# Performance work log

Measured on AMD Instinct MI355X. Metric: run time of the kernel, lower is better.

Reference implementation:

```python
import jax, jax.numpy as jnp
import numpy as np

COMPRESSION = 2

def setup_inputs() -> dict:
    key = jax.random.key(0)
    k = jax.random.split(key, 5)
    B, H, W, C, Ci = 8, 56, 56, 256, 128
    return {
        "x": jax.random.normal(k[0], (B, H, W, C), dtype=jnp.float32),
        "w_theta": jax.random.normal(k[1], (C, Ci), dtype=jnp.float32) * (2.0 / C) ** 0.5,
        "w_phi": jax.random.normal(k[2], (C, Ci), dtype=jnp.float32) * (2.0 / C) ** 0.5,
        "w_g": jax.random.normal(k[3], (C, Ci), dtype=jnp.float32) * (2.0 / C) ** 0.5,
        "w_final": jax.random.normal(k[4], (Ci, C), dtype=jnp.float32) * (2.0 / Ci) ** 0.5,
    }

def _maxpool1d(z, pool):
    # z: [B, N, Ci]; non-overlapping max pool along N (Keras MaxPool1D default stride=pool)
    B, N, Ci = z.shape
    return z[:, : (N // pool) * pool].reshape(B, N // pool, pool, Ci).max(axis=2)

def reference(x, w_theta, w_phi, w_g, w_final):
    B, H, W, C = x.shape
    Ci = w_theta.shape[1]
    N = H * W
    xf = x.reshape(B, N, C)
    # 1x1 convs == per-position matmuls
    theta = xf @ w_theta                      # [B, N, Ci]
    phi = _maxpool1d(xf @ w_phi, COMPRESSION)  # [B, N/2, Ci]
    g = _maxpool1d(xf @ w_g, COMPRESSION)      # [B, N/2, Ci]
    f = jnp.einsum('bnc,bmc->bnm', theta, phi)  # [B, N, N/2]
    f = jax.nn.softmax(f, axis=-1)
    y = jnp.einsum('bnm,bmc->bnc', f, g)        # [B, N, Ci]
    z = y @ w_final                              # [B, N, C]
    return x + z.reshape(B, H, W, C)
```

## Files before the change

kernel.cpp:

```cpp
#include <hip/hip_runtime.h>

typedef _Float16 f16x8 __attribute__((ext_vector_type(8)));
typedef short s16x4 __attribute__((ext_vector_type(4)));
typedef float f32x4 __attribute__((ext_vector_type(4)));

#define MFMA_K32(a, b, c) __builtin_amdgcn_mfma_f32_16x16x32_f16(a, b, c, 0, 0, 0)
#define MFMA_BF(a, b, c)  __builtin_amdgcn_mfma_f32_16x16x16bf16_1k(a, b, c, 0, 0, 0)


__device__ __forceinline__ f16x8 ld8f(const float* __restrict__ p) {
    f32x4 a = *(const f32x4*)p;
    f32x4 b = *(const f32x4*)(p + 4);
    f16x8 r;
    r[0] = (_Float16)a[0]; r[1] = (_Float16)a[1];
    r[2] = (_Float16)a[2]; r[3] = (_Float16)a[3];
    r[4] = (_Float16)b[0]; r[5] = (_Float16)b[1];
    r[6] = (_Float16)b[2]; r[7] = (_Float16)b[3];
    return r;
}
__device__ __forceinline__ unsigned f2bf_rne(float f) {
    unsigned u = __float_as_uint(f);
    return (u + 0x7FFFu + ((u >> 16) & 1u)) >> 16;
}
__device__ __forceinline__ int bfpack_rtz(float lo, float hi) {
    return (int)((__float_as_uint(hi) & 0xFFFF0000u) | (__float_as_uint(lo) >> 16));
}

__global__ void k_prep(const float* __restrict__ wt, const float* __restrict__ wp,
                       const float* __restrict__ wg, const float* __restrict__ wf,
                       _Float16* __restrict__ wt_f, _Float16* __restrict__ wf_f) {
    int i = blockIdx.x * 256 + threadIdx.x;
    int w = i >> 15, idx = i & 32767;
    if (w < 3) {
        const float* src = (w == 0) ? wt : (w == 1) ? wp : wg;
        int k = idx >> 7, n = idx & 127;
        int ct = n >> 4, tt = n & 15, kc = k >> 5, qq = (k >> 3) & 3, jj = k & 7;
        wt_f[((w * 8 + ct) * 8 + kc) * 512 + (qq * 16 + tt) * 8 + jj] = (_Float16)src[idx];
    } else {
        int k = idx >> 8, n = idx & 255;
        int cb = n >> 7, ct = (n >> 4) & 7, tt = n & 15;
        int kc = k >> 5, qq = (k >> 3) & 3, jj = k & 7;
        wf_f[((cb * 8 + ct) * 4 + kc) * 512 + (qq * 16 + tt) * 8 + jj] = (_Float16)wf[idx];
    }
}

__global__ __launch_bounds__(128) void k_proj(
    const float* __restrict__ x,
    const _Float16* __restrict__ wt_f,
    _Float16* __restrict__ theta_f,
    _Float16* __restrict__ phi_f,
    short* __restrict__ g_f)
{
    const int r0   = blockIdx.x * 32;
    const int wave = threadIdx.x >> 6;
    const int lane = threadIdx.x & 63;
    const int q = lane >> 4, t = lane & 15;

    const int mrow = r0 + wave * 16 + t;
    f16x8 af[8];
#pragma unroll
    for (int kc = 0; kc < 8; ++kc)
        af[kc] = ld8f(x + mrow * 256 + kc * 32 + q * 8);

    const f32x4 zero = {0.f, 0.f, 0.f, 0.f};
    f32x4 acc[3][8];
#pragma unroll
    for (int w = 0; w < 3; ++w)
#pragma unroll
        for (int ct = 0; ct < 8; ++ct) acc[w][ct] = zero;

#pragma unroll
    for (int w = 0; w < 3; ++w)
#pragma unroll
        for (int ct = 0; ct < 8; ++ct) {
            const _Float16* Wc = wt_f + ((w * 8 + ct) * 8) * 512 + lane * 8;
#pragma unroll
            for (int kc = 0; kc < 8; ++kc)
                acc[w][ct] = MFMA_K32(af[kc], *(const f16x8*)(Wc + kc * 512), acc[w][ct]);
        }

    _Float16* tb = theta_f + (blockIdx.x * 2 + wave) * 2048;
#pragma unroll
    for (int ct = 0; ct < 8; ++ct) {
        const int off = (ct >> 1) * 512 + ((ct & 1) * 2 + (t >> 3)) * 128 + (t & 7);
#pragma unroll
        for (int r = 0; r < 4; ++r)
            tb[off + (q * 4 + r) * 8] = (_Float16)acc[0][ct][r];
    }

    const int b     = blockIdx.x / 98;
    const int mIdx  = blockIdx.x % 98;
    const int chunk = mIdx >> 1;
    const int h     = mIdx & 1;
    const int ttp   = wave * 8 + q * 2;

    _Float16* pcb = phi_f + (b * 49 + chunk) * 4096;
#pragma unroll
    for (int ct = 0; ct < 8; ++ct) {
        const int kc = ct >> 1;
        const int qq = (ct & 1) * 2 + (t >> 3);
        const int j  = t & 7;
        const int off = (h * 4 + kc) * 512 + (qq * 16 + ttp) * 8 + j;
        pcb[off]     = (_Float16)fmaxf(acc[1][ct][0], acc[1][ct][1]);
        pcb[off + 8] = (_Float16)fmaxf(acc[1][ct][2], acc[1][ct][3]);
    }

    short* gcb = g_f + (b * 49 + chunk) * 4096;
    const int qv  = wave * 2 + (q >> 1);
    const int jj0 = (q & 1) * 2;
#pragma unroll
    for (int ct = 0; ct < 8; ++ct) {
        unsigned lo = f2bf_rne(fmaxf(acc[2][ct][0], acc[2][ct][1]));
        unsigned hi = f2bf_rne(fmaxf(acc[2][ct][2], acc[2][ct][3]));
        *(unsigned*)(gcb + ct * 512 + (qv * 16 + t) * 8 + h * 4 + jj0) = lo | (hi << 16);
    }
}

__global__ __launch_bounds__(256) void k_attn(
    const _Float16* __restrict__ theta_f,
    const _Float16* __restrict__ phi_f,
    const short* __restrict__ g_f,
    _Float16* __restrict__ y_f)
{
    const int blk  = blockIdx.x;
    const int b    = blk & 7;
    const int blkm = blk >> 3;
    const int wave = threadIdx.x >> 6;
    const int lane = threadIdx.x & 63;
    const int q = lane >> 4, t = lane & 15;

    __shared__ __align__(16) _Float16 kv[2][8192];

    const int tIdx = b * 196 + blkm * 4 + wave;
    const _Float16* ph = phi_f + b * 200704;
    const _Float16* gt = (const _Float16*)(g_f + b * 200704);

    f16x8 qf[4];
#pragma unroll
    for (int kc = 0; kc < 4; ++kc)
        qf[kc] = *(const f16x8*)(theta_f + tIdx * 2048 + kc * 512 + lane * 8);

    const f32x4 zero = {0.f, 0.f, 0.f, 0.f};
    f32x4 o[8];
#pragma unroll
    for (int ct = 0; ct < 8; ++ct) o[ct] = zero;
    float lsum = 0.f;
    const float L2E = 1.44269504f, SHIFT = 104.0f;

    const _Float16* src0 = (wave < 2) ? (ph + wave * 2048) : (gt + (wave - 2) * 2048);
    const int doff = wave * 2048;

    f16x8 sr[4];
#pragma unroll
    for (int j = 0; j < 4; ++j)
        sr[j] = *(const f16x8*)(src0 + j * 512 + lane * 8);
#pragma unroll
    for (int j = 0; j < 4; ++j)
        *(f16x8*)(&kv[0][doff + j * 512 + lane * 8]) = sr[j];
    __syncthreads();

    for (int i = 0; i < 49; ++i) {
        if (i + 1 < 49) {
            const _Float16* s = src0 + (i + 1) * 4096;
#pragma unroll
            for (int j = 0; j < 4; ++j)
                sr[j] = *(const f16x8*)(s + j * 512 + lane * 8);
        }

        const _Float16* buf = &kv[i & 1][0];
        f32x4 st0 = zero, st1 = zero;
#pragma unroll
        for (int kc = 0; kc < 4; ++kc) {
            f16x8 a0 = *(const f16x8*)(buf + kc * 512 + lane * 8);
            f16x8 a1 = *(const f16x8*)(buf + (4 + kc) * 512 + lane * 8);
            st0 = MFMA_K32(a0, qf[kc], st0);
            st1 = MFMA_K32(a1, qf[kc], st1);
        }

        f32x4 p0, p1;
#pragma unroll
        for (int r = 0; r < 4; ++r) {
            p0[r] = exp2f(st0[r] * L2E - SHIFT);
            p1[r] = exp2f(st1[r] * L2E - SHIFT);
        }
        lsum += ((p0[0] + p0[1]) + (p0[2] + p0[3]))
              + ((p1[0] + p1[1]) + (p1[2] + p1[3]));
        union { int i2[2]; s16x4 v; } u0, u1;
        u0.i2[0] = bfpack_rtz(p0[0], p0[1]);
        u0.i2[1] = bfpack_rtz(p0[2], p0[3]);
        u1.i2[0] = bfpack_rtz(p1[0], p1[1]);
        u1.i2[1] = bfpack_rtz(p1[2], p1[3]);

#pragma unroll
        for (int ct = 0; ct < 8; ++ct) {
            union { f16x8 f; s16x4 s[2]; } uv;
            uv.f = *(const f16x8*)(buf + 4096 + ct * 512 + lane * 8);
            o[ct] = MFMA_BF(u0.v, uv.s[0], o[ct]);
            o[ct] = MFMA_BF(u1.v, uv.s[1], o[ct]);
        }

        if (i + 1 < 49) {
            _Float16* d = &kv[(i + 1) & 1][doff];
#pragma unroll
            for (int j = 0; j < 4; ++j)
                *(f16x8*)(d + j * 512 + lane * 8) = sr[j];
        }
        __syncthreads();
    }

    float lf = lsum;
    lf += __shfl_xor(lf, 16);
    lf += __shfl_xor(lf, 32);
    float inv[4];
#pragma unroll
    for (int r = 0; r < 4; ++r) inv[r] = 1.0f / __shfl(lf, q * 4 + r);

    _Float16* yb = y_f + tIdx * 2048;
#pragma unroll
    for (int ct = 0; ct < 8; ++ct) {
        const int off = (ct >> 1) * 512 + (2 * (ct & 1) + (t >> 3)) * 128 + (t & 7);
#pragma unroll
        for (int r = 0; r < 4; ++r)
            yb[off + (4 * q + r) * 8] = (_Float16)(o[ct][r] * inv[r]);
    }
}

__global__ __launch_bounds__(256) void k_final(
    const _Float16* __restrict__ y_f,
    const _Float16* __restrict__ wf_f,
    const float* __restrict__ x,
    float* __restrict__ out)
{
    const int r0   = blockIdx.x * 64;
    const int cb   = blockIdx.y;
    const int wave = threadIdx.x >> 6;
    const int lane = threadIdx.x & 63;
    const int q = lane >> 4, t = lane & 15;

    __shared__ float t_lds[4][16][132];

    const int tile = blockIdx.x * 4 + wave;
    f16x8 af[4];
#pragma unroll
    for (int kc = 0; kc < 4; ++kc)
        af[kc] = *(const f16x8*)(y_f + tile * 2048 + kc * 512 + lane * 8);

    const f32x4 zero = {0.f, 0.f, 0.f, 0.f};
    f32x4 acc[8];
#pragma unroll
    for (int ct = 0; ct < 8; ++ct) acc[ct] = zero;
#pragma unroll
    for (int ct = 0; ct < 8; ++ct) {
        const _Float16* Wc = wf_f + ((cb * 8 + ct) * 4) * 512 + lane * 8;
#pragma unroll
        for (int kc = 0; kc < 4; ++kc)
            acc[ct] = MFMA_K32(af[kc], *(const f16x8*)(Wc + kc * 512), acc[ct]);
    }

#pragma unroll
    for (int ct = 0; ct < 8; ++ct)
#pragma unroll
        for (int r = 0; r < 4; ++r)
            t_lds[wave][q * 4 + r][ct * 16 + t] = acc[ct][r];

    const int R0 = r0 + wave * 16;
#pragma unroll
    for (int p = 0; p < 4; ++p) {
        const int rr = p * 4 + q;
        const int c  = t * 8;
        f32x4 v0 = *(const f32x4*)&t_lds[wave][rr][c];
        f32x4 v1 = *(const f32x4*)&t_lds[wave][rr][c + 4];
        const float* xp = x + (R0 + rr) * 256 + cb * 128 + c;
        float* op = out + (R0 + rr) * 256 + cb * 128 + c;
        v0 += *(const f32x4*)xp;
        v1 += *(const f32x4*)(xp + 4);
        *(f32x4*)op = v0;
        *(f32x4*)(op + 4) = v1;
    }
}

extern "C" void kernel_launch(void* const* d_in, const int* in_sizes, int n_in,
                              void* d_out, int out_size, void* d_ws, size_t ws_size,
                              hipStream_t stream) {
    const float* x  = (const float*)d_in[0];
    const float* wt = (const float*)d_in[1];
    const float* wp = (const float*)d_in[2];
    const float* wg = (const float*)d_in[3];
    const float* wf = (const float*)d_in[4];
    float* out = (float*)d_out;

    _Float16* ws      = (_Float16*)d_ws;
    _Float16* wt_f    = ws;
    _Float16* wf_f    = ws + 98304;
    _Float16* theta_f = ws + 131072;
    _Float16* phi_f   = ws + 3342336;
    short*    g_f     = (short*)(ws + 4947968);
    _Float16* y_f     = ws + 6553600;

    k_prep <<<dim3(512),    256, 0, stream>>>(wt, wp, wg, wf, wt_f, wf_f);
    k_proj <<<dim3(784),    128, 0, stream>>>(x, wt_f, theta_f, phi_f, g_f);
    k_attn <<<dim3(392),    256, 0, stream>>>(theta_f, phi_f, g_f, y_f);
    k_final<<<dim3(392, 2), 256, 0, stream>>>(y_f, wf_f, x, out);
}
```

Baseline: 159.6 us.

## Fuse output projection into attention with single-wave blocks holding four query tiles

The attention kernel now runs one wave per block that processes four query tiles. K/V fragments are loaded straight from global memory into registers with software double-buffering, which replaces the shared-memory staging and barriers. The final projection plus residual is fused into the attention epilogue using a transposed f16 weight layout, so the y intermediate buffer and the separate k_final launch go away. The cost is a block count of only 392 single-wave blocks, which leaves many CUs underused. Register pressure is also very high (128 accumulator registers for o plus the q fragments), so spills and latency exposure are a risk.

Result: slower. 186.4 us (+16.8%).

```diff
diff --git a/kernel.cpp b/kernel.cpp
--- a/kernel.cpp
+++ b/kernel.cpp
@@ -1,11 +1,13 @@
 #include <hip/hip_runtime.h>
 
 typedef _Float16 f16x8 __attribute__((ext_vector_type(8)));
+typedef _Float16 f16x4 __attribute__((ext_vector_type(4)));
 typedef short s16x4 __attribute__((ext_vector_type(4)));
 typedef float f32x4 __attribute__((ext_vector_type(4)));
 
 #define MFMA_K32(a, b, c) __builtin_amdgcn_mfma_f32_16x16x32_f16(a, b, c, 0, 0, 0)
 #define MFMA_BF(a, b, c)  __builtin_amdgcn_mfma_f32_16x16x16bf16_1k(a, b, c, 0, 0, 0)
+#define MFMA_F16(a, b, c) __builtin_amdgcn_mfma_f32_16x16x16f16(a, b, c, 0, 0, 0)
 
 
 __device__ __forceinline__ f16x8 ld8f(const float* __restrict__ p) {
@@ -28,7 +30,7 @@
 
 __global__ void k_prep(const float* __restrict__ wt, const float* __restrict__ wp,
                        const float* __restrict__ wg, const float* __restrict__ wf,
-                       _Float16* __restrict__ wt_f, _Float16* __restrict__ wf_f) {
+                       _Float16* __restrict__ wt_f, _Float16* __restrict__ wfT_f) {
     int i = blockIdx.x * 256 + threadIdx.x;
     int w = i >> 15, idx = i & 32767;
     if (w < 3) {
@@ -38,9 +40,9 @@
         wt_f[((w * 8 + ct) * 8 + kc) * 512 + (qq * 16 + tt) * 8 + jj] = (_Float16)src[idx];
     } else {
         int k = idx >> 8, n = idx & 255;
-        int cb = n >> 7, ct = (n >> 4) & 7, tt = n & 15;
-        int kc = k >> 5, qq = (k >> 3) & 3, jj = k & 7;
-        wf_f[((cb * 8 + ct) * 4 + kc) * 512 + (qq * 16 + tt) * 8 + jj] = (_Float16)wf[idx];
+        int ct = n >> 4, tt = n & 15;
+        int kc2 = k >> 4, qq = (k >> 2) & 3, jj = k & 3;
+        wfT_f[ct * 2048 + (qq * 16 + tt) * 32 + kc2 * 4 + jj] = (_Float16)wf[idx];
     }
 }
 
@@ -116,166 +118,123 @@
     }
 }
 
-__global__ __launch_bounds__(256) void k_attn(
+#define LOADKV(DST, SRC) { _Pragma("unroll") \
+    for (int j = 0; j < 8; ++j) DST[j] = *(const f16x8*)((SRC) + j * 512 + lane * 8); }
+
+#define QKSM(PH) { \
+    f32x4 st0[4], st1[4]; \
+    _Pragma("unroll") for (int m = 0; m < 4; ++m) { st0[m] = zero; st1[m] = zero; } \
+    _Pragma("unroll") for (int kc = 0; kc < 4; ++kc) \
+      _Pragma("unroll") for (int m = 0; m < 4; ++m) { \
+        st0[m] = MFMA_K32(PH[kc],     qf[m][kc], st0[m]); \
+        st1[m] = MFMA_K32(PH[4 + kc], qf[m][kc], st1[m]); } \
+    _Pragma("unroll") for (int m = 0; m < 4; ++m) { \
+      f32x4 p0, p1; \
+      _Pragma("unroll") for (int r = 0; r < 4; ++r) { \
+        p0[r] = exp2f(st0[m][r] * L2E - SHIFT); \
+        p1[r] = exp2f(st1[m][r] * L2E - SHIFT); } \
+      lsum[m] += ((p0[0] + p0[1]) + (p0[2] + p0[3])) \
+               + ((p1[0] + p1[1]) + (p1[2] + p1[3])); \
+      u[m][0].i2[0] = bfpack_rtz(p0[0], p0[1]); \
+      u[m][0].i2[1] = bfpack_rtz(p0[2], p0[3]); \
+      u[m][1].i2[0] = bfpack_rtz(p1[0], p1[1]); \
+      u[m][1].i2[1] = bfpack_rtz(p1[2], p1[3]); } }
+
+#define PV(AG) { \
+    _Pragma("unroll") for (int ct = 0; ct < 8; ++ct) { \
+      union { f16x8 f; s16x4 s[2]; } uv; uv.f = AG[ct]; \
+      _Pragma("unroll") for (int m = 0; m < 4; ++m) { \
+        o[m][ct] = MFMA_BF(uv.s[0], u[m][0].v, o[m][ct]); \
+        o[m][ct] = MFMA_BF(uv.s[1], u[m][1].v, o[m][ct]); } } }
+
+__global__ __launch_bounds__(64, 1) void k_attn(
     const _Float16* __restrict__ theta_f,
     const _Float16* __restrict__ phi_f,
     const short* __restrict__ g_f,
-    _Float16* __restrict__ y_f)
+    const _Float16* __restrict__ wfT_f,
+    const float* __restrict__ x,
+    float* __restrict__ out)
 {
     const int blk  = blockIdx.x;
     const int b    = blk & 7;
     const int blkm = blk >> 3;
-    const int wave = threadIdx.x >> 6;
     const int lane = threadIdx.x & 63;
     const int q = lane >> 4, t = lane & 15;
 
-    __shared__ __align__(16) _Float16 kv[2][8192];
-
-    const int tIdx = b * 196 + blkm * 4 + wave;
+    const int tIdx0 = b * 196 + blkm * 4;
     const _Float16* ph = phi_f + b * 200704;
     const _Float16* gt = (const _Float16*)(g_f + b * 200704);
 
-    f16x8 qf[4];
-#pragma unroll
-    for (int kc = 0; kc < 4; ++kc)
-        qf[kc] = *(const f16x8*)(theta_f + tIdx * 2048 + kc * 512 + lane * 8);
+    f16x8 qf[4][4];
+#pragma unroll
+    for (int m = 0; m < 4; ++m)
+#pragma unroll
+        for (int kc = 0; kc < 4; ++kc)
+            qf[m][kc] = *(const f16x8*)(theta_f + (tIdx0 + m) * 2048 + kc * 512 + lane * 8);
 
     const f32x4 zero = {0.f, 0.f, 0.f, 0.f};
-    f32x4 o[8];
-#pragma unroll
-    for (int ct = 0; ct < 8; ++ct) o[ct] = zero;
-    float lsum = 0.f;
+    f32x4 o[4][8];
+#pragma unroll
+    for (int m = 0; m < 4; ++m)
+#pragma unroll
+        for (int ct = 0; ct < 8; ++ct) o[m][ct] = zero;
+    float lsum[4] = {0.f, 0.f, 0.f, 0.f};
+    union ubf { int i2[2]; s16x4 v; } u[4][2];
     const float L2E = 1.44269504f, SHIFT = 104.0f;
 
-    const _Float16* src0 = (wave < 2) ? (ph + wave * 2048) : (gt + (wave - 2) * 2048);
-    const int doff = wave * 2048;
-
-    f16x8 sr[4];
-#pragma unroll
-    for (int j = 0; j < 4; ++j)
-        sr[j] = *(const f16x8*)(src0 + j * 512 + lane * 8);
-#pragma unroll
-    for (int j = 0; j < 4; ++j)
-        *(f16x8*)(&kv[0][doff + j * 512 + lane * 8]) = sr[j];
-    __syncthreads();
-
-    for (int i = 0; i < 49; ++i) {
-        if (i + 1 < 49) {
-            const _Float16* s = src0 + (i + 1) * 4096;
-#pragma unroll
-            for (int j = 0; j < 4; ++j)
-                sr[j] = *(const f16x8*)(s + j * 512 + lane * 8);
+    f16x8 phA[8], phB[8], ag[8];
+    LOADKV(phA, ph);
+
+#pragma unroll 1
+    for (int i = 0; i < 48; i += 2) {
+        LOADKV(ag, gt + i * 4096);
+        QKSM(phA);
+        LOADKV(phB, ph + (i + 1) * 4096);
+        PV(ag);
+        LOADKV(ag, gt + (i + 1) * 4096);
+        QKSM(phB);
+        LOADKV(phA, ph + (i + 2) * 4096);
+        PV(ag);
+    }
+    LOADKV(ag, gt + 48 * 4096);
+    QKSM(phA);
+    PV(ag);
+
+    float inv[4];
+#pragma unroll
+    for (int m = 0; m < 4; ++m) {
+        float lf = lsum[m];
+        lf += __shfl_xor(lf, 16);
+        lf += __shfl_xor(lf, 32);
+        inv[m] = 1.0f / lf;
+    }
+
+    f16x4 yf[4][8];
+#pragma unroll
+    for (int m = 0; m < 4; ++m)
+#pragma unroll
+        for (int ct = 0; ct < 8; ++ct)
+#pragma unroll
+            for (int r = 0; r < 4; ++r)
+                yf[m][ct][r] = (_Float16)(o[m][ct][r] * inv[m]);
+
+    const int row0 = tIdx0 * 16;
+    for (int ctile = 0; ctile < 16; ++ctile) {
+        union { f16x8 v8; f16x4 v4[2]; } w[4];
+#pragma unroll
+        for (int p = 0; p < 4; ++p)
+            w[p].v8 = *(const f16x8*)(wfT_f + ctile * 2048 + lane * 32 + p * 8);
+#pragma unroll
+        for (int m = 0; m < 4; ++m) {
+            f32x4 acc = zero;
+#pragma unroll
+            for (int kc2 = 0; kc2 < 8; ++kc2)
+                acc = MFMA_F16(w[kc2 >> 1].v4[kc2 & 1], yf[m][kc2], acc);
+            const int row = row0 + m * 16 + t;
+            const int col = ctile * 16 + q * 4;
+            f32x4 xv = *(const f32x4*)(x + row * 256 + col);
+            *(f32x4*)(out + row * 256 + col) = acc + xv;
         }
-
-        const _Float16* buf = &kv[i & 1][0];
-        f32x4 st0 = zero, st1 = zero;
-#pragma unroll
-        for (int kc = 0; kc < 4; ++kc) {
-            f16x8 a0 = *(const f16x8*)(buf + kc * 512 + lane * 8);
-            f16x8 a1 = *(const f16x8*)(buf + (4 + kc) * 512 + lane * 8);
-            st0 = MFMA_K32(a0, qf[kc], st0);
-            st1 = MFMA_K32(a1, qf[kc], st1);
-        }
-
-        f32x4 p0, p1;
-#pragma unroll
-        for (int r = 0; r < 4; ++r) {
-            p0[r] = exp2f(st0[r] * L2E - SHIFT);
-            p1[r] = exp2f(st1[r] * L2E - SHIFT);
-        }
-        lsum += ((p0[0] + p0[1]) + (p0[2] + p0[3]))
-              + ((p1[0] + p1[1]) + (p1[2] + p1[3]));
-        union { int i2[2]; s16x4 v; } u0, u1;
-        u0.i2[0] = bfpack_rtz(p0[0], p0[1]);
-        u0.i2[1] = bfpack_rtz(p0[2], p0[3]);
-        u1.i2[0] = bfpack_rtz(p1[0], p1[1]);
-        u1.i2[1] = bfpack_rtz(p1[2], p1[3]);
-
-#pragma unroll
-        for (int ct = 0; ct < 8; ++ct) {
-            union { f16x8 f; s16x4 s[2]; } uv;
-            uv.f = *(const f16x8*)(buf + 4096 + ct * 512 + lane * 8);
-            o[ct] = MFMA_BF(u0.v, uv.s[0], o[ct]);
-            o[ct] = MFMA_BF(u1.v, uv.s[1], o[ct]);
-        }
-
-        if (i + 1 < 49) {
-            _Float16* d = &kv[(i + 1) & 1][doff];
-#pragma unroll
-            for (int j = 0; j < 4; ++j)
-                *(f16x8*)(d + j * 512 + lane * 8) = sr[j];
-        }
-        __syncthreads();
-    }
-
-    float lf = lsum;
-    lf += __shfl_xor(lf, 16);
-    lf += __shfl_xor(lf, 32);
-    float inv[4];
-#pragma unroll
-    for (int r = 0; r < 4; ++r) inv[r] = 1.0f / __shfl(lf, q * 4 + r);
-
-    _Float16* yb = y_f + tIdx * 2048;
-#pragma unroll
-    for (int ct = 0; ct < 8; ++ct) {
-        const int off = (ct >> 1) * 512 + (2 * (ct & 1) + (t >> 3)) * 128 + (t & 7);
-#pragma unroll
-        for (int r = 0; r < 4; ++r)
-            yb[off + (4 * q + r) * 8] = (_Float16)(o[ct][r] * inv[r]);
-    }
-}
-
-__global__ __launch_bounds__(256) void k_final(
-    const _Float16* __restrict__ y_f,
-    const _Float16* __restrict__ wf_f,
-    const float* __restrict__ x,
-    float* __restrict__ out)
-{
-    const int r0   = blockIdx.x * 64;
-    const int cb   = blockIdx.y;
-    const int wave = threadIdx.x >> 6;
-    const int lane = threadIdx.x & 63;
-    const int q = lane >> 4, t = lane & 15;
-
-    __shared__ float t_lds[4][16][132];
-
-    const int tile = blockIdx.x * 4 + wave;
-    f16x8 af[4];
-#pragma unroll
-    for (int kc = 0; kc < 4; ++kc)
-        af[kc] = *(const f16x8*)(y_f + tile * 2048 + kc * 512 + lane * 8);
-
-    const f32x4 zero = {0.f, 0.f, 0.f, 0.f};
-    f32x4 acc[8];
-#pragma unroll
-    for (int ct = 0; ct < 8; ++ct) acc[ct] = zero;
-#pragma unroll
-    for (int ct = 0; ct < 8; ++ct) {
-        const _Float16* Wc = wf_f + ((cb * 8 + ct) * 4) * 512 + lane * 8;
-#pragma unroll
-        for (int kc = 0; kc < 4; ++kc)
-            acc[ct] = MFMA_K32(af[kc], *(const f16x8*)(Wc + kc * 512), acc[ct]);
-    }
-
-#pragma unroll
-    for (int ct = 0; ct < 8; ++ct)
-#pragma unroll
-        for (int r = 0; r < 4; ++r)
-            t_lds[wave][q * 4 + r][ct * 16 + t] = acc[ct][r];
-
-    const int R0 = r0 + wave * 16;
-#pragma unroll
-    for (int p = 0; p < 4; ++p) {
-        const int rr = p * 4 + q;
-        const int c  = t * 8;
-        f32x4 v0 = *(const f32x4*)&t_lds[wave][rr][c];
-        f32x4 v1 = *(const f32x4*)&t_lds[wave][rr][c + 4];
-        const float* xp = x + (R0 + rr) * 256 + cb * 128 + c;
-        float* op = out + (R0 + rr) * 256 + cb * 128 + c;
-        v0 += *(const f32x4*)xp;
-        v1 += *(const f32x4*)(xp + 4);
-        *(f32x4*)op = v0;
-        *(f32x4*)(op + 4) = v1;
     }
 }
 
@@ -291,14 +250,12 @@
 
     _Float16* ws      = (_Float16*)d_ws;
     _Float16* wt_f    = ws;
-    _Float16* wf_f    = ws + 98304;
+    _Float16* wfT_f   = ws + 98304;
     _Float16* theta_f = ws + 131072;
     _Float16* phi_f   = ws + 3342336;
     short*    g_f     = (short*)(ws + 4947968);
-    _Float16* y_f     = ws + 6553600;
-
-    k_prep <<<dim3(512),    256, 0, stream>>>(wt, wp, wg, wf, wt_f, wf_f);
-    k_proj <<<dim3(784),    128, 0, stream>>>(x, wt_f, theta_f, phi_f, g_f);
-    k_attn <<<dim3(392),    256, 0, stream>>>(theta_f, phi_f, g_f, y_f);
-    k_final<<<dim3(392, 2), 256, 0, stream>>>(y_f, wf_f, x, out);
-}
+
+    k_prep<<<dim3(512), 256, 0, stream>>>(wt, wp, wg, wf, wt_f, wfT_f);
+    k_proj<<<dim3(784), 128, 0, stream>>>(x, wt_f, theta_f, phi_f, g_f);
+    k_attn<<<dim3(392),  64, 0, stream>>>(theta_f, phi_f, g_f, wfT_f, x, out);
+}
```

## Fuse final projection and residual into attention kernel; split projection per weight

Applied to the files above, without the earlier changes.

The final 1x1 projection and residual add move into the end of the attention kernel. The PV MFMA operands are swapped so the normalized output tile already sits in registers in the B-operand layout, and it is multiplied by a transposed f16 w_final. This removes the y intermediate round trip through global memory and one kernel launch. The projection kernel also now assigns one weight (theta, phi or g) per wave instead of all three, giving three times as many waves with fewer accumulators each. The risks are that the attention kernel's tail gets longer and runs with only 392 blocks, and that x is reloaded with 16-byte row-strided accesses.

New measurement: 160.4 us. About the same (+0.5%).

```diff
diff --git a/kernel.cpp b/kernel.cpp
--- a/kernel.cpp
+++ b/kernel.cpp
@@ -1,11 +1,13 @@
 #include <hip/hip_runtime.h>
 
 typedef _Float16 f16x8 __attribute__((ext_vector_type(8)));
+typedef _Float16 f16x4 __attribute__((ext_vector_type(4)));
 typedef short s16x4 __attribute__((ext_vector_type(4)));
 typedef float f32x4 __attribute__((ext_vector_type(4)));
 
 #define MFMA_K32(a, b, c) __builtin_amdgcn_mfma_f32_16x16x32_f16(a, b, c, 0, 0, 0)
 #define MFMA_BF(a, b, c)  __builtin_amdgcn_mfma_f32_16x16x16bf16_1k(a, b, c, 0, 0, 0)
+#define MFMA_F16(a, b, c) __builtin_amdgcn_mfma_f32_16x16x16f16(a, b, c, 0, 0, 0)
 
 
 __device__ __forceinline__ f16x8 ld8f(const float* __restrict__ p) {
@@ -28,7 +30,7 @@
 
 __global__ void k_prep(const float* __restrict__ wt, const float* __restrict__ wp,
                        const float* __restrict__ wg, const float* __restrict__ wf,
-                       _Float16* __restrict__ wt_f, _Float16* __restrict__ wf_f) {
+                       _Float16* __restrict__ wt_f, _Float16* __restrict__ wfT_f) {
     int i = blockIdx.x * 256 + threadIdx.x;
     int w = i >> 15, idx = i & 32767;
     if (w < 3) {
@@ -38,81 +40,85 @@
         wt_f[((w * 8 + ct) * 8 + kc) * 512 + (qq * 16 + tt) * 8 + jj] = (_Float16)src[idx];
     } else {
         int k = idx >> 8, n = idx & 255;
-        int cb = n >> 7, ct = (n >> 4) & 7, tt = n & 15;
-        int kc = k >> 5, qq = (k >> 3) & 3, jj = k & 7;
-        wf_f[((cb * 8 + ct) * 4 + kc) * 512 + (qq * 16 + tt) * 8 + jj] = (_Float16)wf[idx];
-    }
-}
-
-__global__ __launch_bounds__(128) void k_proj(
+        int ct = n >> 4, tt = n & 15;
+        int kc2 = k >> 4, qq = (k >> 2) & 3, jj = k & 3;
+        wfT_f[ct * 2048 + (qq * 16 + tt) * 32 + kc2 * 4 + jj] = (_Float16)wf[idx];
+    }
+}
+
+__global__ __launch_bounds__(256) void k_proj(
     const float* __restrict__ x,
     const _Float16* __restrict__ wt_f,
     _Float16* __restrict__ theta_f,
     _Float16* __restrict__ phi_f,
     short* __restrict__ g_f)
 {
-    const int r0   = blockIdx.x * 32;
-    const int wave = threadIdx.x >> 6;
+    const int u    = blockIdx.x * 4 + (threadIdx.x >> 6);
     const int lane = threadIdx.x & 63;
     const int q = lane >> 4, t = lane & 15;
 
-    const int mrow = r0 + wave * 16 + t;
+    const int tt = u / 3;
+    const int w  = u - tt * 3;
+
+    const int mrow = tt * 16 + t;
     f16x8 af[8];
 #pragma unroll
     for (int kc = 0; kc < 8; ++kc)
         af[kc] = ld8f(x + mrow * 256 + kc * 32 + q * 8);
 
     const f32x4 zero = {0.f, 0.f, 0.f, 0.f};
-    f32x4 acc[3][8];
-#pragma unroll
-    for (int w = 0; w < 3; ++w)
-#pragma unroll
-        for (int ct = 0; ct < 8; ++ct) acc[w][ct] = zero;
-
-#pragma unroll
-    for (int w = 0; w < 3; ++w)
-#pragma unroll
-        for (int ct = 0; ct < 8; ++ct) {
-            const _Float16* Wc = wt_f + ((w * 8 + ct) * 8) * 512 + lane * 8;
-#pragma unroll
-            for (int kc = 0; kc < 8; ++kc)
-                acc[w][ct] = MFMA_K32(af[kc], *(const f16x8*)(Wc + kc * 512), acc[w][ct]);
-        }
-
-    _Float16* tb = theta_f + (blockIdx.x * 2 + wave) * 2048;
+    f32x4 acc[8];
+#pragma unroll
+    for (int ct = 0; ct < 8; ++ct) acc[ct] = zero;
+
 #pragma unroll
     for (int ct = 0; ct < 8; ++ct) {
-        const int off = (ct >> 1) * 512 + ((ct & 1) * 2 + (t >> 3)) * 128 + (t & 7);
-#pragma unroll
-        for (int r = 0; r < 4; ++r)
-            tb[off + (q * 4 + r) * 8] = (_Float16)acc[0][ct][r];
-    }
-
-    const int b     = blockIdx.x / 98;
-    const int mIdx  = blockIdx.x % 98;
-    const int chunk = mIdx >> 1;
-    const int h     = mIdx & 1;
-    const int ttp   = wave * 8 + q * 2;
-
-    _Float16* pcb = phi_f + (b * 49 + chunk) * 4096;
-#pragma unroll
-    for (int ct = 0; ct < 8; ++ct) {
-        const int kc = ct >> 1;
-        const int qq = (ct & 1) * 2 + (t >> 3);
-        const int j  = t & 7;
-        const int off = (h * 4 + kc) * 512 + (qq * 16 + ttp) * 8 + j;
-        pcb[off]     = (_Float16)fmaxf(acc[1][ct][0], acc[1][ct][1]);
-        pcb[off + 8] = (_Float16)fmaxf(acc[1][ct][2], acc[1][ct][3]);
-    }
-
-    short* gcb = g_f + (b * 49 + chunk) * 4096;
-    const int qv  = wave * 2 + (q >> 1);
-    const int jj0 = (q & 1) * 2;
-#pragma unroll
-    for (int ct = 0; ct < 8; ++ct) {
-        unsigned lo = f2bf_rne(fmaxf(acc[2][ct][0], acc[2][ct][1]));
-        unsigned hi = f2bf_rne(fmaxf(acc[2][ct][2], acc[2][ct][3]));
-        *(unsigned*)(gcb + ct * 512 + (qv * 16 + t) * 8 + h * 4 + jj0) = lo | (hi << 16);
+        const _Float16* Wc = wt_f + ((w * 8 + ct) * 8) * 512 + lane * 8;
+#pragma unroll
+        for (int kc = 0; kc < 8; ++kc)
+            acc[ct] = MFMA_K32(af[kc], *(const f16x8*)(Wc + kc * 512), acc[ct]);
+    }
+
+    if (w == 0) {
+        _Float16* tb = theta_f + tt * 2048;
+#pragma unroll
+        for (int ct = 0; ct < 8; ++ct) {
+            const int off = (ct >> 1) * 512 + ((ct & 1) * 2 + (t >> 3)) * 128 + (t & 7);
+#pragma unroll
+            for (int r = 0; r < 4; ++r)
+                tb[off + (q * 4 + r) * 8] = (_Float16)acc[ct][r];
+        }
+        return;
+    }
+
+    const int b     = tt / 196;
+    const int tl    = tt - b * 196;
+    const int chunk = tl >> 2;
+    const int sub   = tl & 3;
+    const int h     = sub >> 1;
+
+    if (w == 1) {
+        const int ttp = (sub & 1) * 8 + q * 2;
+        _Float16* pcb = phi_f + (b * 49 + chunk) * 4096;
+#pragma unroll
+        for (int ct = 0; ct < 8; ++ct) {
+            const int kc = ct >> 1;
+            const int qq = (ct & 1) * 2 + (t >> 3);
+            const int j  = t & 7;
+            const int off = (h * 4 + kc) * 512 + (qq * 16 + ttp) * 8 + j;
+            pcb[off]     = (_Float16)fmaxf(acc[ct][0], acc[ct][1]);
+            pcb[off + 8] = (_Float16)fmaxf(acc[ct][2], acc[ct][3]);
+        }
+    } else {
+        short* gcb = g_f + (b * 49 + chunk) * 4096;
+        const int qv  = (sub & 1) * 2 + (q >> 1);
+        const int jj0 = (q & 1) * 2;
+#pragma unroll
+        for (int ct = 0; ct < 8; ++ct) {
+            unsigned lo = f2bf_rne(fmaxf(acc[ct][0], acc[ct][1]));
+            unsigned hi = f2bf_rne(fmaxf(acc[ct][2], acc[ct][3]));
+            *(unsigned*)(gcb + ct * 512 + (qv * 16 + t) * 8 + h * 4 + jj0) = lo | (hi << 16);
+        }
     }
 }
 
@@ -120,7 +126,9 @@
     const _Float16* __restrict__ theta_f,
     const _Float16* __restrict__ phi_f,
     const short* __restrict__ g_f,
-    _Float16* __restrict__ y_f)
+    const _Float16* __restrict__ wfT_f,
+    const float* __restrict__ x,
+    float* __restrict__ out)
 {
     const int blk  = blockIdx.x;
     const int b    = blk & 7;
@@ -195,8 +203,8 @@
         for (int ct = 0; ct < 8; ++ct) {
             union { f16x8 f; s16x4 s[2]; } uv;
             uv.f = *(const f16x8*)(buf + 4096 + ct * 512 + lane * 8);
-            o[ct] = MFMA_BF(u0.v, uv.s[0], o[ct]);
-            o[ct] = MFMA_BF(u1.v, uv.s[1], o[ct]);
+            o[ct] = MFMA_BF(uv.s[0], u0.v, o[ct]);
+            o[ct] = MFMA_BF(uv.s[1], u1.v, o[ct]);
         }
 
         if (i + 1 < 49) {
@@ -211,71 +219,29 @@
     float lf = lsum;
     lf += __shfl_xor(lf, 16);
     lf += __shfl_xor(lf, 32);
-    float inv[4];
-#pragma unroll
-    for (int r = 0; r < 4; ++r) inv[r] = 1.0f / __shfl(lf, q * 4 + r);
-
-    _Float16* yb = y_f + tIdx * 2048;
-#pragma unroll
-    for (int ct = 0; ct < 8; ++ct) {
-        const int off = (ct >> 1) * 512 + (2 * (ct & 1) + (t >> 3)) * 128 + (t & 7);
+    const float inv = 1.0f / lf;
+
+    f16x4 yf[8];
+#pragma unroll
+    for (int ct = 0; ct < 8; ++ct)
 #pragma unroll
         for (int r = 0; r < 4; ++r)
-            yb[off + (4 * q + r) * 8] = (_Float16)(o[ct][r] * inv[r]);
-    }
-}
-
-__global__ __launch_bounds__(256) void k_final(
-    const _Float16* __restrict__ y_f,
-    const _Float16* __restrict__ wf_f,
-    const float* __restrict__ x,
-    float* __restrict__ out)
-{
-    const int r0   = blockIdx.x * 64;
-    const int cb   = blockIdx.y;
-    const int wave = threadIdx.x >> 6;
-    const int lane = threadIdx.x & 63;
-    const int q = lane >> 4, t = lane & 15;
-
-    __shared__ float t_lds[4][16][132];
-
-    const int tile = blockIdx.x * 4 + wave;
-    f16x8 af[4];
-#pragma unroll
-    for (int kc = 0; kc < 4; ++kc)
-        af[kc] = *(const f16x8*)(y_f + tile * 2048 + kc * 512 + lane * 8);
-
-    const f32x4 zero = {0.f, 0.f, 0.f, 0.f};
-    f32x4 acc[8];
-#pragma unroll
-    for (int ct = 0; ct < 8; ++ct) acc[ct] = zero;
-#pragma unroll
-    for (int ct = 0; ct < 8; ++ct) {
-        const _Float16* Wc = wf_f + ((cb * 8 + ct) * 4) * 512 + lane * 8;
-#pragma unroll
-        for (int kc = 0; kc < 4; ++kc)
-            acc[ct] = MFMA_K32(af[kc], *(const f16x8*)(Wc + kc * 512), acc[ct]);
-    }
-
-#pragma unroll
-    for (int ct = 0; ct < 8; ++ct)
-#pragma unroll
-        for (int r = 0; r < 4; ++r)
-            t_lds[wave][q * 4 + r][ct * 16 + t] = acc[ct][r];
-
-    const int R0 = r0 + wave * 16;
-#pragma unroll
-    for (int p = 0; p < 4; ++p) {
-        const int rr = p * 4 + q;
-        const int c  = t * 8;
-        f32x4 v0 = *(const f32x4*)&t_lds[wave][rr][c];
-        f32x4 v1 = *(const f32x4*)&t_lds[wave][rr][c + 4];
-        const float* xp = x + (R0 + rr) * 256 + cb * 128 + c;
-        float* op = out + (R0 + rr) * 256 + cb * 128 + c;
-        v0 += *(const f32x4*)xp;
-        v1 += *(const f32x4*)(xp + 4);
-        *(f32x4*)op = v0;
-        *(f32x4*)(op + 4) = v1;
+            yf[ct][r] = (_Float16)(o[ct][r] * inv);
+
+    const int row = tIdx * 16 + t;
+#pragma unroll 1
+    for (int ctile = 0; ctile < 16; ++ctile) {
+        union { f16x8 v8; f16x4 v4[2]; } w[4];
+#pragma unroll
+        for (int p = 0; p < 4; ++p)
+            w[p].v8 = *(const f16x8*)(wfT_f + ctile * 2048 + lane * 32 + p * 8);
+        f32x4 acc = zero;
+#pragma unroll
+        for (int kc2 = 0; kc2 < 8; ++kc2)
+            acc = MFMA_F16(w[kc2 >> 1].v4[kc2 & 1], yf[kc2], acc);
+        const int col = ctile * 16 + q * 4;
+        f32x4 xv = *(const f32x4*)(x + row * 256 + col);
+        *(f32x4*)(out + row * 256 + col) = acc + xv;
     }
 }
 
@@ -291,14 +257,12 @@
 
     _Float16* ws      = (_Float16*)d_ws;
     _Float16* wt_f    = ws;
-    _Float16* wf_f    = ws + 98304;
+    _Float16* wfT_f   = ws + 98304;
     _Float16* theta_f = ws + 131072;
     _Float16* phi_f   = ws + 3342336;
     short*    g_f     = (short*)(ws + 4947968);
-    _Float16* y_f     = ws + 6553600;
-
-    k_prep <<<dim3(512),    256, 0, stream>>>(wt, wp, wg, wf, wt_f, wf_f);
-    k_proj <<<dim3(784),    128, 0, stream>>>(x, wt_f, theta_f, phi_f, g_f);
-    k_attn <<<dim3(392),    256, 0, stream>>>(theta_f, phi_f, g_f, y_f);
-    k_final<<<dim3(392, 2), 256, 0, stream>>>(y_f, wf_f, x, out);
-}
+
+    k_prep<<<dim3(512),  256, 0, stream>>>(wt, wp, wg, wf, wt_f, wfT_f);
+    k_proj<<<dim3(1176), 256, 0, stream>>>(x, wt_f, theta_f, phi_f, g_f);
+    k_attn<<<dim3(392),  256, 0, stream>>>(theta_f, phi_f, g_f, wfT_f, x, out);
+}
```
